# Performance work log

Hardware: AMD Instinct MI355X
Metric: run time of the kernel (lower is better)

## Reference

```python
import jax, jax.numpy as jnp
import numpy as np

EPS = 1e-5


def setup_inputs() -> dict:
    key = jax.random.key(0)
    ks = jax.random.split(key, 7)
    B, T, H = 4, 4096, 1024
    x = jax.random.normal(ks[0], (B, T, H), dtype=jnp.float32)
    gamma = jnp.ones((H,), dtype=jnp.float32)
    beta = jnp.zeros((H,), dtype=jnp.float32)
    s = 1.0 / np.sqrt(H)
    Wg = jax.random.uniform(ks[1], (H, H), minval=-s, maxval=s, dtype=jnp.float32)
    bg = jax.random.uniform(ks[2], (H,), minval=-s, maxval=s, dtype=jnp.float32)
    Wc = jax.random.uniform(ks[3], (H, H), minval=-s, maxval=s, dtype=jnp.float32)
    bc = jax.random.uniform(ks[4], (H,), minval=-s, maxval=s, dtype=jnp.float32)
    return {"x": x, "gamma": gamma, "beta": beta, "Wg": Wg, "bg": bg, "Wc": Wc, "bc": bc}


def reference(x, gamma, beta, Wg, bg, Wc, bc):
    # x: [B, T, H]
    mu = jnp.mean(x, axis=-1, keepdims=True)
    var = jnp.mean((x - mu) ** 2, axis=-1, keepdims=True)
    normed = (x - mu) * jax.lax.rsqrt(var + EPS) * gamma + beta
    z = jax.nn.sigmoid(jnp.einsum('bth,oh->bto', normed, Wg) + bg)  # gate
    c = jnp.einsum('bth,oh->bto', normed, Wc) + bc                  # candidate
    B, T, H = x.shape

    def step(h, zc):
        z_t, c_t = zc  # each [B, H]
        h = (1.0 - z_t) * h + z_t * c_t
        return h, h

    h0 = jnp.zeros((B, H), dtype=x.dtype)
    # scan over time: move T to leading axis
    _, hs = jax.lax.scan(step, h0, (jnp.swapaxes(z, 0, 1), jnp.swapaxes(c, 0, 1)))
    return jnp.swapaxes(hs, 0, 1) + x  # residual
```

## Files before the change

### kernel.cpp

```cpp
#include <hip/hip_runtime.h>
#include <stdint.h>


#define B_    4
#define T_    4096
#define H_    1024
#define BT_   (B_*T_)
#define EPSV  1e-5f
#define CHK   256
#define CL    (T_/CHK)
#define BM    256
#define BN    128
#define BK    32

typedef float  f32x4  __attribute__((ext_vector_type(4)));
typedef __bf16 bf16x8 __attribute__((ext_vector_type(8)));
typedef unsigned short u16;

__device__ __forceinline__ u16 f2bf(float f) {
  uint32_t u = __builtin_bit_cast(uint32_t, f);
  u += 0x7fffu + ((u >> 16) & 1u);
  return (u16)(u >> 16);
}
__device__ __forceinline__ float bf2f(uint32_t u) {
  uint32_t v = (u & 0xffffu) << 16;
  return __builtin_bit_cast(float, v);
}
__device__ __forceinline__ void bf4(uint2 p, float* f) {
  f[0] = bf2f(p.x); f[1] = bf2f(p.x >> 16);
  f[2] = bf2f(p.y); f[3] = bf2f(p.y >> 16);
}

__global__ __launch_bounds__(256) void ln_kernel(
    const float* __restrict__ x, const float* __restrict__ gamma,
    const float* __restrict__ beta, u16* __restrict__ normed) {
  const int wid  = threadIdx.x >> 6, lane = threadIdx.x & 63;
  const int row  = blockIdx.x * 4 + wid;
  const float4* xr = reinterpret_cast<const float4*>(x + (size_t)row * H_);
  float4 v[4];
  float s = 0.0f, q = 0.0f;
  #pragma unroll
  for (int seg = 0; seg < 4; ++seg) {
    v[seg] = xr[seg * 64 + lane];
    s += v[seg].x + v[seg].y + v[seg].z + v[seg].w;
    q += v[seg].x*v[seg].x + v[seg].y*v[seg].y + v[seg].z*v[seg].z + v[seg].w*v[seg].w;
  }
  #pragma unroll
  for (int off = 1; off < 64; off <<= 1) {
    s += __shfl_xor(s, off);
    q += __shfl_xor(q, off);
  }
  const float mean = s * (1.0f / H_);
  const float var  = q * (1.0f / H_) - mean * mean;
  const float rstd = rsqrtf(var + EPSV);
  const float4* g4 = reinterpret_cast<const float4*>(gamma);
  const float4* b4 = reinterpret_cast<const float4*>(beta);
  uint2* o2 = reinterpret_cast<uint2*>(normed + (size_t)row * H_);
  #pragma unroll
  for (int seg = 0; seg < 4; ++seg) {
    const float4 g = g4[seg * 64 + lane];
    const float4 b = b4[seg * 64 + lane];
    uint2 o;
    o.x = (uint32_t)f2bf((v[seg].x - mean) * rstd * g.x + b.x)
        | ((uint32_t)f2bf((v[seg].y - mean) * rstd * g.y + b.y) << 16);
    o.y = (uint32_t)f2bf((v[seg].z - mean) * rstd * g.z + b.z)
        | ((uint32_t)f2bf((v[seg].w - mean) * rstd * g.w + b.w) << 16);
    o2[seg * 64 + lane] = o;
  }
}

__global__ __launch_bounds__(256) void pack_kernel(
    const float* __restrict__ Wg, const float* __restrict__ Wc,
    u16* __restrict__ wpack) {
  const int idx4 = (blockIdx.x * 256 + threadIdx.x) * 4;
  const int n = idx4 >> 10;
  const int k = idx4 & 1023;
  const float* src = (n < 1024) ? (Wg + (size_t)n * 1024 + k)
                                : (Wc + (size_t)(n - 1024) * 1024 + k);
  const float4 v = *reinterpret_cast<const float4*>(src);
  uint2 o;
  o.x = (uint32_t)f2bf(v.x) | ((uint32_t)f2bf(v.y) << 16);
  o.y = (uint32_t)f2bf(v.z) | ((uint32_t)f2bf(v.w) << 16);
  *reinterpret_cast<uint2*>(wpack + idx4) = o;
}

__global__ __launch_bounds__(256, 2) void gemm_kernel(
    const u16* __restrict__ A, const u16* __restrict__ Bw,
    const float* __restrict__ bg, const float* __restrict__ bc,
    u16* __restrict__ zbuf, u16* __restrict__ cbuf) {
  __shared__ u16 As[2][BM * BK];
  __shared__ u16 Bs[2][BN * BK];
  const int bid = blockIdx.x;
  const int nb  = (bid & 7) * 128 + (bid >> 3);
  const int mt  = nb >> 4, nt = nb & 15;
  const int tid = threadIdx.x;
  const int wid = tid >> 6, lane = tid & 63;
  const int wr  = wid >> 1, wcq = wid & 1;
  const int frow = lane & 15;
  const int physslot = (lane >> 4) ^ ((frow >> 1) & 3);

  f32x4 acc[8][4] = {};

  const u16* aptr[4];
  const u16* bptr[2];
  #pragma unroll
  for (int i = 0; i < 4; ++i) {
    const int c = tid + 256 * i;
    const int row = c >> 2;
    const int sl = (c & 3) ^ ((row >> 1) & 3);
    aptr[i] = A + (size_t)(mt * BM + row) * 1024 + sl * 8;
  }
  #pragma unroll
  for (int i = 0; i < 2; ++i) {
    const int c = tid + 256 * i;
    const int row = c >> 2;
    const int sl = (c & 3) ^ ((row >> 1) & 3);
    bptr[i] = Bw + (size_t)(nt * BN + row) * 1024 + sl * 8;
  }

  auto stage = [&](int buf, int ks) {
    const int kk = ks * BK;
    #pragma unroll
    for (int i = 0; i < 4; ++i)
      __builtin_amdgcn_global_load_lds(
          (const __attribute__((address_space(1))) void*)(aptr[i] + kk),
          (__attribute__((address_space(3))) void*)&As[buf][(tid + 256 * i) * 8], 16, 0, 0);
    #pragma unroll
    for (int i = 0; i < 2; ++i)
      __builtin_amdgcn_global_load_lds(
          (const __attribute__((address_space(1))) void*)(bptr[i] + kk),
          (__attribute__((address_space(3))) void*)&Bs[buf][(tid + 256 * i) * 8], 16, 0, 0);
  };
  auto compute = [&](int buf) {
    bf16x8 bfr[4];
    #pragma unroll
    for (int n = 0; n < 4; ++n)
      bfr[n] = *reinterpret_cast<const bf16x8*>(
          &Bs[buf][(wcq * 64 + n * 16 + frow) * BK + physslot * 8]);
    #pragma unroll
    for (int m = 0; m < 8; ++m) {
      const bf16x8 am = *reinterpret_cast<const bf16x8*>(
          &As[buf][(wr * 128 + m * 16 + frow) * BK + physslot * 8]);
      #pragma unroll
      for (int n = 0; n < 4; ++n)
        acc[m][n] = __builtin_amdgcn_mfma_f32_16x16x32_bf16(am, bfr[n], acc[m][n], 0, 0, 0);
    }
  };

  stage(0, 0);
  __syncthreads();
  int cur = 0;
  for (int ks = 0; ks < 31; ++ks) {
    stage(cur ^ 1, ks + 1);
    compute(cur);
    __syncthreads();
    cur ^= 1;
  }
  compute(cur);

  const int r0 = (lane >> 4) * 4;
  const int col16 = lane & 15;
  const bool isz = (nt < 8);
  #pragma unroll
  for (int m = 0; m < 8; ++m) {
    #pragma unroll
    for (int n = 0; n < 4; ++n) {
      const int col = nt * BN + wcq * 64 + n * 16 + col16;
      #pragma unroll
      for (int r = 0; r < 4; ++r) {
        const int row = mt * BM + wr * 128 + m * 16 + r0 + r;
        float v = acc[m][n][r];
        if (isz) {
          v += bg[col];
          v = 1.0f / (1.0f + __expf(-v));
          zbuf[(size_t)row * 1024 + col] = f2bf(v);
        } else {
          const int cc = col - 1024;
          v += bc[cc];
          cbuf[(size_t)row * 1024 + cc] = f2bf(v);
        }
      }
    }
  }
}

__global__ __launch_bounds__(256) void scan1_kernel(
    const u16* __restrict__ zbuf, const u16* __restrict__ cbuf,
    float* __restrict__ Achk, float* __restrict__ Uchk) {
  const int bid   = blockIdx.x;
  const int chunk = bid & (CHK - 1);
  const int b     = bid >> 8;
  const int o4    = threadIdx.x * 4;
  const size_t base = ((size_t)(b * T_ + chunk * CL)) * H_ + o4;
  float A[4] = {1.f, 1.f, 1.f, 1.f};
  float u[4] = {0.f, 0.f, 0.f, 0.f};
  #pragma unroll
  for (int t = 0; t < CL; ++t) {
    const size_t idx = base + (size_t)t * H_;
    const uint2 zp = *reinterpret_cast<const uint2*>(&zbuf[idx]);
    const uint2 cp = *reinterpret_cast<const uint2*>(&cbuf[idx]);
    float z[4], c[4];
    bf4(zp, z); bf4(cp, c);
    #pragma unroll
    for (int j = 0; j < 4; ++j) {
      const float a = 1.0f - z[j];
      A[j] *= a;
      u[j] = a * u[j] + z[j] * c[j];
    }
  }
  const int idx = (b * CHK + chunk) * H_ + o4;
  *reinterpret_cast<float4*>(&Achk[idx]) = make_float4(A[0], A[1], A[2], A[3]);
  *reinterpret_cast<float4*>(&Uchk[idx]) = make_float4(u[0], u[1], u[2], u[3]);
}

__global__ __launch_bounds__(256) void scan2_kernel(
    const float* __restrict__ Achk, const float* __restrict__ Uchk,
    float* __restrict__ Hin) {
  const int g = blockIdx.x * 256 + threadIdx.x;
  const int b = g >> 10;
  const int o = g & 1023;
  float h = 0.0f;
  #pragma unroll 8
  for (int j = 0; j < CHK; ++j) {
    const int idx = (b * CHK + j) * H_ + o;
    Hin[idx] = h;
    h = Achk[idx] * h + Uchk[idx];
  }
}

__global__ __launch_bounds__(256) void scan3_kernel(
    const u16* __restrict__ zbuf, const u16* __restrict__ cbuf,
    const float* __restrict__ Hin, const float* __restrict__ x,
    float* __restrict__ out) {
  const int bid   = blockIdx.x;
  const int chunk = bid & (CHK - 1);
  const int b     = bid >> 8;
  const int o4    = threadIdx.x * 4;
  const float4 hv = *reinterpret_cast<const float4*>(&Hin[(b * CHK + chunk) * H_ + o4]);
  float h[4] = {hv.x, hv.y, hv.z, hv.w};
  const size_t base = ((size_t)(b * T_ + chunk * CL)) * H_ + o4;
  #pragma unroll
  for (int t = 0; t < CL; ++t) {
    const size_t idx = base + (size_t)t * H_;
    const uint2 zp = *reinterpret_cast<const uint2*>(&zbuf[idx]);
    const uint2 cp = *reinterpret_cast<const uint2*>(&cbuf[idx]);
    const float4 xv = *reinterpret_cast<const float4*>(&x[idx]);
    float z[4], c[4];
    bf4(zp, z); bf4(cp, c);
    #pragma unroll
    for (int j = 0; j < 4; ++j)
      h[j] = (1.0f - z[j]) * h[j] + z[j] * c[j];
    *reinterpret_cast<float4*>(&out[idx]) =
        make_float4(h[0] + xv.x, h[1] + xv.y, h[2] + xv.z, h[3] + xv.w);
  }
}

extern "C" void kernel_launch(void* const* d_in, const int* in_sizes, int n_in,
                              void* d_out, int out_size, void* d_ws, size_t ws_size,
                              hipStream_t stream) {
  const float* x     = (const float*)d_in[0];
  const float* gamma = (const float*)d_in[1];
  const float* beta  = (const float*)d_in[2];
  const float* Wg    = (const float*)d_in[3];
  const float* bg    = (const float*)d_in[4];
  const float* Wc    = (const float*)d_in[5];
  const float* bc    = (const float*)d_in[6];
  float* out = (float*)d_out;

  char* ws = (char*)d_ws;
  u16*   normed = (u16*)(ws);
  u16*   wpack  = (u16*)(ws + 33554432ull);
  u16*   zbuf   = (u16*)(ws + 37748736ull);
  u16*   cbuf   = (u16*)(ws + 71303168ull);
  float* Achk   = (float*)(ws);
  float* Uchk   = (float*)(ws + 4194304ull);
  float* Hin    = (float*)(ws + 8388608ull);

  ln_kernel  <<<BT_/4, 256, 0, stream>>>(x, gamma, beta, normed);
  pack_kernel<<<2048,  256, 0, stream>>>(Wg, Wc, wpack);
  gemm_kernel<<<1024,  256, 0, stream>>>(normed, wpack, bg, bc, zbuf, cbuf);
  scan1_kernel<<<B_*CHK, 256, 0, stream>>>(zbuf, cbuf, Achk, Uchk);
  scan2_kernel<<<16,     256, 0, stream>>>(Achk, Uchk, Hin);
  scan3_kernel<<<B_*CHK, 256, 0, stream>>>(zbuf, cbuf, Hin, x, out);
}
```

Baseline: 319.8 us.

## Parallelize chunk-carry scan hierarchically and deepen GEMM LDS pipeline with raw waitcnt

The serial 256-step carry scan, which ran on only 16 blocks, becomes a two-level scan. 16 lanes per channel each fold 16 chunks and then run a shuffle-based prefix. scan3 then replays up to 15 chunk carries per block from Achk/Uchk, which adds some redundant loads. The GEMM main loop also now keeps two stages in flight, using explicit s_waitcnt vmcnt and s_barrier in place of __syncthreads. This hides global-load latency but depends on the vmcnt count matching the number of loads issued per stage.

```diff
diff --git a/kernel.cpp b/kernel.cpp
--- a/kernel.cpp
+++ b/kernel.cpp
@@ -9,6 +9,7 @@
 #define EPSV  1e-5f
 #define CHK   256
 #define CL    (T_/CHK)
+#define NG    16
 #define BM    256
 #define BN    128
 #define BK    32
@@ -16,6 +17,9 @@
 typedef float  f32x4  __attribute__((ext_vector_type(4)));
 typedef __bf16 bf16x8 __attribute__((ext_vector_type(8)));
 typedef unsigned short u16;
+
+#define ASM_VMCNT(N) asm volatile("s_waitcnt vmcnt(" #N ")" ::: "memory")
+#define ASM_BAR()    asm volatile("s_barrier" ::: "memory")
 
 __device__ __forceinline__ u16 f2bf(float f) {
   uint32_t u = __builtin_bit_cast(uint32_t, f);
@@ -148,14 +152,21 @@
   };
 
   stage(0, 0);
-  __syncthreads();
+  stage(1, 1);
   int cur = 0;
-  for (int ks = 0; ks < 31; ++ks) {
-    stage(cur ^ 1, ks + 1);
+  for (int ks = 0; ks < 30; ++ks) {
+    ASM_VMCNT(6);
+    ASM_BAR();
     compute(cur);
-    __syncthreads();
+    ASM_BAR();
+    stage(cur, ks + 2);
     cur ^= 1;
   }
+  ASM_VMCNT(6);  ASM_BAR();
+  compute(cur);
+  ASM_BAR();
+  cur ^= 1;
+  ASM_VMCNT(0);  ASM_BAR();
   compute(cur);
 
   const int r0 = (lane >> 4) * 4;
@@ -213,31 +224,61 @@
   *reinterpret_cast<float4*>(&Uchk[idx]) = make_float4(u[0], u[1], u[2], u[3]);
 }
 
-__global__ __launch_bounds__(256) void scan2_kernel(
+__global__ __launch_bounds__(256) void scan2ab_kernel(
     const float* __restrict__ Achk, const float* __restrict__ Uchk,
-    float* __restrict__ Hin) {
-  const int g = blockIdx.x * 256 + threadIdx.x;
-  const int b = g >> 10;
-  const int o = g & 1023;
-  float h = 0.0f;
-  #pragma unroll 8
-  for (int j = 0; j < CHK; ++j) {
-    const int idx = (b * CHK + j) * H_ + o;
-    Hin[idx] = h;
-    h = Achk[idx] * h + Uchk[idx];
-  }
+    float* __restrict__ Hgrp) {
+  const int t    = blockIdx.x * 256 + threadIdx.x;
+  const int b    = t >> 14;
+  const int idx  = t & 16383;
+  const int o    = idx >> 4;
+  const int g    = idx & 15;
+  const int lane = threadIdx.x & 63;
+
+  float A = 1.0f, u = 0.0f;
+  #pragma unroll
+  for (int c = 0; c < 16; ++c) {
+    const int chunk = g * 16 + c;
+    const int e = (b * CHK + chunk) * H_ + o;
+    const float a = Achk[e];
+    u = a * u + Uchk[e];
+    A *= a;
+  }
+  #pragma unroll
+  for (int d = 1; d < 16; d <<= 1) {
+    const float Ap = __shfl_up(A, d, 16);
+    const float up = __shfl_up(u, d, 16);
+    if ((lane & 15) >= d) {
+      u = A * up + u;
+      A = A * Ap;
+    }
+  }
+  const float hg = __shfl_up(u, 1, 16);
+  Hgrp[(b * NG + g) * H_ + o] = (g == 0) ? 0.0f : hg;
 }
 
 __global__ __launch_bounds__(256) void scan3_kernel(
     const u16* __restrict__ zbuf, const u16* __restrict__ cbuf,
-    const float* __restrict__ Hin, const float* __restrict__ x,
+    const float* __restrict__ Achk, const float* __restrict__ Uchk,
+    const float* __restrict__ Hgrp, const float* __restrict__ x,
     float* __restrict__ out) {
   const int bid   = blockIdx.x;
   const int chunk = bid & (CHK - 1);
   const int b     = bid >> 8;
+  const int g     = chunk >> 4;
   const int o4    = threadIdx.x * 4;
-  const float4 hv = *reinterpret_cast<const float4*>(&Hin[(b * CHK + chunk) * H_ + o4]);
+
+  float4 hv = *reinterpret_cast<const float4*>(&Hgrp[(b * NG + g) * H_ + o4]);
   float h[4] = {hv.x, hv.y, hv.z, hv.w};
+  for (int jc = g * 16; jc < chunk; ++jc) {
+    const int e = (b * CHK + jc) * H_ + o4;
+    const float4 a4 = *reinterpret_cast<const float4*>(&Achk[e]);
+    const float4 u4 = *reinterpret_cast<const float4*>(&Uchk[e]);
+    h[0] = a4.x * h[0] + u4.x;
+    h[1] = a4.y * h[1] + u4.y;
+    h[2] = a4.z * h[2] + u4.z;
+    h[3] = a4.w * h[3] + u4.w;
+  }
+
   const size_t base = ((size_t)(b * T_ + chunk * CL)) * H_ + o4;
   #pragma unroll
   for (int t = 0; t < CL; ++t) {
@@ -274,12 +315,12 @@
   u16*   cbuf   = (u16*)(ws + 71303168ull);
   float* Achk   = (float*)(ws);
   float* Uchk   = (float*)(ws + 4194304ull);
-  float* Hin    = (float*)(ws + 8388608ull);
+  float* Hgrp   = (float*)(ws + 8388608ull);
 
   ln_kernel  <<<BT_/4, 256, 0, stream>>>(x, gamma, beta, normed);
   pack_kernel<<<2048,  256, 0, stream>>>(Wg, Wc, wpack);
   gemm_kernel<<<1024,  256, 0, stream>>>(normed, wpack, bg, bc, zbuf, cbuf);
-  scan1_kernel<<<B_*CHK, 256, 0, stream>>>(zbuf, cbuf, Achk, Uchk);
-  scan2_kernel<<<16,     256, 0, stream>>>(Achk, Uchk, Hin);
-  scan3_kernel<<<B_*CHK, 256, 0, stream>>>(zbuf, cbuf, Hin, x, out);
-}
+  scan1_kernel <<<B_*CHK, 256, 0, stream>>>(zbuf, cbuf, Achk, Uchk);
+  scan2ab_kernel<<<(B_*H_*NG)/256, 256, 0, stream>>>(Achk, Uchk, Hgrp);
+  scan3_kernel <<<B_*CHK, 256, 0, stream>>>(zbuf, cbuf, Achk, Uchk, Hgrp, x, out);
+}
```

Result: faster. 291.4 us (-8.9%).
